# Performance work log

Hardware: AMD Instinct MI355X
Metric: run time of the kernel (lower is better)

Reference implementation:

```python
import jax, jax.numpy as jnp
import numpy as np

N_NODES = 65536
N_EDGES = 1048576
D_IN = 1024
D_HID = 64
N_CLS = 32


def gcn_conv(x, W, b, src, dst, n_nodes):
    """PyG GCNConv: linear transform, then symmetric-normalized aggregation
    with implicit self-loops (fill value 1)."""
    xw = x @ W  # [N, d_out]
    e = src.shape[0]
    # degree over destination index, including the self-loop (+1)
    deg = jax.ops.segment_sum(jnp.ones((e,), xw.dtype), dst, num_segments=n_nodes) + 1.0
    dinv_sqrt = jax.lax.rsqrt(deg)  # deg >= 1, safe
    norm = dinv_sqrt[src] * dinv_sqrt[dst]  # [E]
    agg = jax.ops.segment_sum(xw[src] * norm[:, None], dst, num_segments=n_nodes)
    # self-loop contribution: norm = deg_i^{-1}
    agg = agg + xw * (1.0 / deg)[:, None]
    return agg + b


def setup_inputs() -> dict:
    key = jax.random.key(0)
    k_x, k_e, k_w1, k_b1, k_w2, k_b2 = jax.random.split(key, 6)
    x = jax.random.normal(k_x, (N_NODES, D_IN), dtype=jnp.float32)
    edge_index = jax.random.randint(k_e, (2, N_EDGES), 0, N_NODES, dtype=jnp.int64)
    s1 = 1.0 / np.sqrt(D_IN)
    s2 = 1.0 / np.sqrt(D_HID)
    W1 = jax.random.uniform(k_w1, (D_IN, D_HID), jnp.float32, -s1, s1)
    b1 = jax.random.uniform(k_b1, (D_HID,), jnp.float32, -s1, s1)
    W2 = jax.random.uniform(k_w2, (D_HID, N_CLS), jnp.float32, -s2, s2)
    b2 = jax.random.uniform(k_b2, (N_CLS,), jnp.float32, -s2, s2)
    return {"x": x, "edge_index": edge_index, "W1": W1, "b1": b1, "W2": W2, "b2": b2}


def reference(x, edge_index, W1, b1, W2, b2):
    src, dst = edge_index[0], edge_index[1]
    n = x.shape[0]
    h = gcn_conv(x, W1, b1, src, dst, n)
    h = jax.nn.relu(h)
    # dropout is identity in eval mode
    h = gcn_conv(h, W2, b2, src, dst, n)
    return jax.nn.log_softmax(h, axis=1)
```

## Files before the change

### kernel.cpp

```cpp
#include <hip/hip_runtime.h>
#include <hip/hip_bf16.h>

#define N_NODES 65536
#define D_IN 1024
#define D_HID 64
#define N_CLS 32
#define CPAD 5

typedef short short8 __attribute__((ext_vector_type(8)));
typedef float floatx4 __attribute__((ext_vector_type(4)));

__device__ __forceinline__ unsigned short f2bf(float f) {
  union { float f; unsigned u; } cv; cv.f = f;
  unsigned r = (cv.u + 0x7FFFu + ((cv.u >> 16) & 1u)) >> 16;
  return (unsigned short)r;
}
__device__ __forceinline__ float2 bf2f2(unsigned v) {
  union { unsigned u; float f; } a, b;
  a.u = v << 16;
  b.u = v & 0xFFFF0000u;
  return make_float2(a.f, b.f);
}

__global__ void k_count_w1t(const int* __restrict__ dst, int* __restrict__ cnt,
                            const float* __restrict__ w1, unsigned short* __restrict__ w1t,
                            int e4) {
  int b = blockIdx.x;
  if (b >= 1024) {
    int i = (b - 1024) * 256 + threadIdx.x;
    int k = i / D_HID, n = i % D_HID;
    w1t[n * D_IN + k] = f2bf(w1[i]);
    return;
  }
  int i = b * 256 + threadIdx.x;
  if (i < e4) {
    int4 d = ((const int4*)dst)[i];
    atomicAdd(&cnt[d.x << CPAD], 1);
    atomicAdd(&cnt[d.y << CPAD], 1);
    atomicAdd(&cnt[d.z << CPAD], 1);
    atomicAdd(&cnt[d.w << CPAD], 1);
  }
}

__global__ void k_scan_a(const int* __restrict__ cnt, int* __restrict__ bsum) {
  __shared__ int s[256];
  int t = threadIdx.x;
  s[t] = cnt[(blockIdx.x * 256 + t) << CPAD];
  __syncthreads();
  for (int off = 128; off > 0; off >>= 1) {
    if (t < off) s[t] += s[t + off];
    __syncthreads();
  }
  if (t == 0) bsum[blockIdx.x] = s[0];
}

__global__ void k_scan_c(const int* __restrict__ cnt, const int* __restrict__ bsum,
                         int* __restrict__ rowptr, int* __restrict__ cursor,
                         float* __restrict__ dinv) {
  __shared__ int s[256];
  int t = threadIdx.x;
  s[t] = (t < blockIdx.x) ? bsum[t] : 0;
  __syncthreads();
  for (int off = 128; off > 0; off >>= 1) {
    if (t < off) s[t] += s[t + off];
    __syncthreads();
  }
  int blockoff = s[0];
  __syncthreads();
  int i = blockIdx.x * 256 + t;
  int v = cnt[i << CPAD];
  s[t] = v;
  __syncthreads();
  for (int off = 1; off < 256; off <<= 1) {
    int x = (t >= off) ? s[t - off] : 0;
    __syncthreads();
    s[t] += x;
    __syncthreads();
  }
  int excl = s[t] - v + blockoff;
  rowptr[i] = excl;
  cursor[i << CPAD] = excl;
  dinv[i] = rsqrtf((float)(v + 1));
  if (i == N_NODES - 1) rowptr[N_NODES] = excl + v;
}

__global__ __launch_bounds__(256) void k_fill_gemm1(
    const int* __restrict__ src, const int* __restrict__ dst,
    int* __restrict__ cursor, int* __restrict__ csr_src, int e4,
    const float* __restrict__ x, const unsigned short* __restrict__ w1t,
    const float* __restrict__ dinv, unsigned short* __restrict__ xw1s) {
  if (blockIdx.x >= 1024) {
    int i = (blockIdx.x - 1024) * 256 + threadIdx.x;
    int e8 = e4 >> 1;
    if (i < e8) {
      const int4* d4 = (const int4*)dst;
      const int4* s4 = (const int4*)src;
      int4 da = d4[2 * i], db = d4[2 * i + 1];
      int4 sa = s4[2 * i], sb = s4[2 * i + 1];
      int p0 = atomicAdd(&cursor[da.x << CPAD], 1);
      int p1 = atomicAdd(&cursor[da.y << CPAD], 1);
      int p2 = atomicAdd(&cursor[da.z << CPAD], 1);
      int p3 = atomicAdd(&cursor[da.w << CPAD], 1);
      int p4 = atomicAdd(&cursor[db.x << CPAD], 1);
      int p5 = atomicAdd(&cursor[db.y << CPAD], 1);
      int p6 = atomicAdd(&cursor[db.z << CPAD], 1);
      int p7 = atomicAdd(&cursor[db.w << CPAD], 1);
      csr_src[p0] = sa.x; csr_src[p1] = sa.y;
      csr_src[p2] = sa.z; csr_src[p3] = sa.w;
      csr_src[p4] = sb.x; csr_src[p5] = sb.y;
      csr_src[p6] = sb.z; csr_src[p7] = sb.w;
    }
    return;
  }
  int wave = threadIdx.x >> 6;
  int lane = threadIdx.x & 63;
  int quad = lane >> 4;
  int l16 = lane & 15;
  int rowbase = blockIdx.x * 64 + wave * 16;
  const float* xrow = x + (size_t)(rowbase + l16) * D_IN + quad * 8;
  const unsigned short* bbase = w1t + quad * 8;
  floatx4 acc[4];
#pragma unroll
  for (int nt = 0; nt < 4; nt++) acc[nt] = (floatx4){0.f, 0.f, 0.f, 0.f};
  float4 p0 = *(const float4*)(xrow + 0);
  float4 p1 = *(const float4*)(xrow + 4);
  float4 p2 = *(const float4*)(xrow + 32);
  float4 p3 = *(const float4*)(xrow + 36);
  short8 bf0[4], bf1[4];
#pragma unroll
  for (int nt = 0; nt < 4; nt++) {
    const unsigned short* bp = bbase + (size_t)(nt * 16 + l16) * D_IN;
    bf0[nt] = *(const short8*)(bp);
    bf1[nt] = *(const short8*)(bp + 32);
  }
  for (int k0 = 0; k0 < D_IN; k0 += 64) {
    float4 c0 = p0, c1 = p1, c2 = p2, c3 = p3;
    int kn = (k0 + 64 < D_IN) ? k0 + 64 : k0;
    p0 = *(const float4*)(xrow + kn);
    p1 = *(const float4*)(xrow + kn + 4);
    p2 = *(const float4*)(xrow + kn + 32);
    p3 = *(const float4*)(xrow + kn + 36);
    float av0[8] = {c0.x, c0.y, c0.z, c0.w, c1.x, c1.y, c1.z, c1.w};
    float av1[8] = {c2.x, c2.y, c2.z, c2.w, c3.x, c3.y, c3.z, c3.w};
    short8 af0, af1;
    unsigned* u0 = (unsigned*)&af0;
    unsigned* u1 = (unsigned*)&af1;
#pragma unroll
    for (int j = 0; j < 4; j++) {
      asm("v_cvt_pk_bf16_f32 %0, %1, %2" : "=v"(u0[j]) : "v"(av0[2 * j]), "v"(av0[2 * j + 1]));
      asm("v_cvt_pk_bf16_f32 %0, %1, %2" : "=v"(u1[j]) : "v"(av1[2 * j]), "v"(av1[2 * j + 1]));
    }
#pragma unroll
    for (int nt = 0; nt < 4; nt++)
      acc[nt] = __builtin_amdgcn_mfma_f32_16x16x32_bf16(af0, bf0[nt], acc[nt], 0, 0, 0);
#pragma unroll
    for (int nt = 0; nt < 4; nt++)
      bf0[nt] = *(const short8*)(bbase + (size_t)(nt * 16 + l16) * D_IN + kn);
#pragma unroll
    for (int nt = 0; nt < 4; nt++)
      acc[nt] = __builtin_amdgcn_mfma_f32_16x16x32_bf16(af1, bf1[nt], acc[nt], 0, 0, 0);
#pragma unroll
    for (int nt = 0; nt < 4; nt++)
      bf1[nt] = *(const short8*)(bbase + (size_t)(nt * 16 + l16) * D_IN + kn + 32);
  }
#pragma unroll
  for (int r = 0; r < 4; r++) {
    int row = rowbase + quad * 4 + r;
    float sc = dinv[row];
#pragma unroll
    for (int nt = 0; nt < 4; nt++)
      xw1s[(size_t)row * D_HID + nt * 16 + l16] = f2bf(acc[nt][r] * sc);
  }
}

__global__ __launch_bounds__(256) void k_agg1(const unsigned* __restrict__ xw1s2,
    const int* __restrict__ rowptr, const int* __restrict__ csr_src,
    const float* __restrict__ dinv, const float* __restrict__ b1,
    const float* __restrict__ w2, unsigned short* __restrict__ xw2s) {
  __shared__ float w2s[D_HID * N_CLS];
  for (int i = threadIdx.x; i < D_HID * N_CLS; i += 256) w2s[i] = w2[i];
  __syncthreads();
  int wave = threadIdx.x >> 6;
  int lane = threadIdx.x & 63;
  int h = lane >> 5, l = lane & 31;
  int node = blockIdx.x * 4 + wave;
  float dd = dinv[node];
  int beg = rowptr[node], end = rowptr[node + 1];
  float cx[8], cy[8];
#pragma unroll
  for (int j = 0; j < 8; j++) { cx[j] = 0.f; cy[j] = 0.f; }
  for (int e = beg + h; e < end; e += 16) {
    int idx[8]; bool val[8];
#pragma unroll
    for (int j = 0; j < 8; j++) {
      int ee = e + 2 * j;
      val[j] = ee < end;
      idx[j] = csr_src[val[j] ? ee : beg];
    }
#pragma unroll
    for (int j = 0; j < 8; j++) {
      float2 v = bf2f2(xw1s2[(size_t)idx[j] * 32 + l]);
      cx[j] += val[j] ? v.x : 0.f;
      cy[j] += val[j] ? v.y : 0.f;
    }
  }
  float sx = ((cx[0] + cx[1]) + (cx[2] + cx[3])) + ((cx[4] + cx[5]) + (cx[6] + cx[7]));
  float sy = ((cy[0] + cy[1]) + (cy[2] + cy[3])) + ((cy[4] + cy[5]) + (cy[6] + cy[7]));
  sx += __shfl_xor(sx, 32);
  sy += __shfl_xor(sy, 32);
  float2 self = bf2f2(xw1s2[(size_t)node * 32 + l]);
  float2 bb = ((const float2*)b1)[l];
  float vx = dd * (sx + self.x) + bb.x;
  float vy = dd * (sy + self.y) + bb.y;
  vx = vx > 0.f ? vx : 0.f;
  vy = vy > 0.f ? vy : 0.f;
  int c = lane & 31;
  float p = 0.f;
#pragma unroll
  for (int kk = 0; kk < 32; kk++) {
    int k = h * 32 + kk;
    float hv = (k & 1) ? __shfl(vy, k >> 1) : __shfl(vx, k >> 1);
    p += hv * w2s[k * N_CLS + c];
  }
  p += __shfl_xor(p, 32);
  if (lane < 32) xw2s[(size_t)node * N_CLS + c] = f2bf(p * dd);
}

__global__ __launch_bounds__(256) void k_agg2(const unsigned* __restrict__ xw2s2,
    const int* __restrict__ rowptr, const int* __restrict__ csr_src,
    const float* __restrict__ dinv, const float* __restrict__ b2,
    float* __restrict__ out) {
  int wave = threadIdx.x >> 6;
  int lane = threadIdx.x & 63;
  int q = lane >> 4, l = lane & 15;
  int node = blockIdx.x * 4 + wave;
  float dd = dinv[node];
  int beg = rowptr[node], end = rowptr[node + 1];
  float cx[4], cy[4];
#pragma unroll
  for (int j = 0; j < 4; j++) { cx[j] = 0.f; cy[j] = 0.f; }
  for (int e = beg + q; e < end; e += 16) {
    int idx[4]; bool val[4];
#pragma unroll
    for (int j = 0; j < 4; j++) {
      int ee = e + 4 * j;
      val[j] = ee < end;
      idx[j] = csr_src[val[j] ? ee : beg];
    }
#pragma unroll
    for (int j = 0; j < 4; j++) {
      float2 v = bf2f2(xw2s2[(size_t)idx[j] * 16 + l]);
      cx[j] += val[j] ? v.x : 0.f;
      cy[j] += val[j] ? v.y : 0.f;
    }
  }
  float sx = (cx[0] + cx[1]) + (cx[2] + cx[3]);
  float sy = (cy[0] + cy[1]) + (cy[2] + cy[3]);
  sx += __shfl_xor(sx, 32); sy += __shfl_xor(sy, 32);
  sx += __shfl_xor(sx, 16); sy += __shfl_xor(sy, 16);
  float2 self = bf2f2(xw2s2[(size_t)node * 16 + l]);
  float2 bb = ((const float2*)b2)[l];
  float lx = dd * (sx + self.x) + bb.x;
  float ly = dd * (sy + self.y) + bb.y;
  float m = fmaxf(lx, ly);
#pragma unroll
  for (int o = 8; o > 0; o >>= 1) m = fmaxf(m, __shfl_xor(m, o));
  float s2 = __expf(lx - m) + __expf(ly - m);
#pragma unroll
  for (int o = 8; o > 0; o >>= 1) s2 += __shfl_xor(s2, o);
  float lse = m + __logf(s2);
  if (lane < 16)
    ((float2*)out)[(size_t)node * 16 + l] = make_float2(lx - lse, ly - lse);
}

extern "C" void kernel_launch(void* const* d_in, const int* in_sizes, int n_in,
                              void* d_out, int out_size, void* d_ws, size_t ws_size,
                              hipStream_t stream) {
  (void)n_in; (void)out_size; (void)ws_size;
  const float* x  = (const float*)d_in[0];
  const int*   ei = (const int*)d_in[1];
  const float* w1 = (const float*)d_in[2];
  const float* b1 = (const float*)d_in[3];
  const float* w2 = (const float*)d_in[4];
  const float* b2 = (const float*)d_in[5];
  float* out = (float*)d_out;
  int e = in_sizes[1] / 2;
  const int* src = ei;
  const int* dst = ei + e;

  char* ws = (char*)d_ws;
  int* cnt            = (int*)(ws + 0x0000000);
  int* cursor         = (int*)(ws + 0x0800000);
  int* rowptr         = (int*)(ws + 0x1000000);
  float* dinv         = (float*)(ws + 0x1050000);
  int* bsum           = (int*)(ws + 0x1090000);
  int* csr_src        = (int*)(ws + 0x10A0000);
  unsigned short* w1t = (unsigned short*)(ws + 0x14A0000);
  unsigned short* xw1s= (unsigned short*)(ws + 0x14C0000);
  unsigned short* xw2s= (unsigned short*)(ws + 0x1CC0000);

  int e4 = e / 4;
  hipMemsetAsync(cnt, 0, (size_t)N_NODES * 32 * sizeof(int), stream);
  k_count_w1t<<<1280, 256, 0, stream>>>(dst, cnt, w1, w1t, e4);
  k_scan_a   <<<N_NODES / 256, 256, 0, stream>>>(cnt, bsum);
  k_scan_c   <<<N_NODES / 256, 256, 0, stream>>>(cnt, bsum, rowptr, cursor, dinv);
  k_fill_gemm1<<<1536, 256, 0, stream>>>(src, dst, cursor, csr_src, e4,
                                         x, w1t, dinv, xw1s);
  k_agg1     <<<N_NODES / 4, 256, 0, stream>>>((const unsigned*)xw1s, rowptr, csr_src,
                                               dinv, b1, w2, xw2s);
  k_agg2     <<<N_NODES / 4, 256, 0, stream>>>((const unsigned*)xw2s, rowptr, csr_src,
                                               dinv, b2, out);
}
```

Before: 549.1 us.

## Build CSR with two-level bucketed counting sort using shared-memory atomics

Replaces the global-atomic degree count and cursor-based CSR fill with a two-pass bucket sort. Edges are histogrammed by the high bits of dst into 256 buckets using per-block shared-memory atomics, then scattered as packed (dst low byte, src) words. A per-bucket kernel then builds rowptr, dinv and csr_src locally. This removes the large padded counter memset and the contended random global atomics. In exchange the CSR build now takes more kernel launches, and the first GEMM no longer overlaps with the edge fill. Packing src into 16 bits relies on there being at most 65536 nodes.

Measured after the change: 493.9 us. -10.1%, faster.

```diff
diff --git a/kernel.cpp b/kernel.cpp
--- a/kernel.cpp
+++ b/kernel.cpp
@@ -5,7 +5,8 @@
 #define D_IN 1024
 #define D_HID 64
 #define N_CLS 32
-#define CPAD 5
+#define NBUK 256
+#define NEB 1024
 
 typedef short short8 __attribute__((ext_vector_type(8)));
 typedef float floatx4 __attribute__((ext_vector_type(4)));
@@ -22,53 +23,55 @@
   return make_float2(a.f, b.f);
 }
 
-__global__ void k_count_w1t(const int* __restrict__ dst, int* __restrict__ cnt,
-                            const float* __restrict__ w1, unsigned short* __restrict__ w1t,
-                            int e4) {
+__global__ void k_hist(const int* __restrict__ dst, int* __restrict__ H,
+                       const float* __restrict__ w1, unsigned short* __restrict__ w1t,
+                       int e4) {
   int b = blockIdx.x;
-  if (b >= 1024) {
-    int i = (b - 1024) * 256 + threadIdx.x;
+  if (b >= NEB) {
+    int i = (b - NEB) * 256 + threadIdx.x;
     int k = i / D_HID, n = i % D_HID;
     w1t[n * D_IN + k] = f2bf(w1[i]);
     return;
   }
-  int i = b * 256 + threadIdx.x;
-  if (i < e4) {
-    int4 d = ((const int4*)dst)[i];
-    atomicAdd(&cnt[d.x << CPAD], 1);
-    atomicAdd(&cnt[d.y << CPAD], 1);
-    atomicAdd(&cnt[d.z << CPAD], 1);
-    atomicAdd(&cnt[d.w << CPAD], 1);
-  }
-}
-
-__global__ void k_scan_a(const int* __restrict__ cnt, int* __restrict__ bsum) {
+  __shared__ int hist[NBUK];
+  int t = threadIdx.x;
+  hist[t] = 0;
+  __syncthreads();
+  int i4 = b * 256 + t;
+  if (i4 < e4) {
+    int4 d = ((const int4*)dst)[i4];
+    atomicAdd(&hist[d.x >> 8], 1);
+    atomicAdd(&hist[d.y >> 8], 1);
+    atomicAdd(&hist[d.z >> 8], 1);
+    atomicAdd(&hist[d.w >> 8], 1);
+  }
+  __syncthreads();
+  H[t * NEB + b] = hist[t];
+}
+
+__global__ void k_scan_bucket(int* __restrict__ H, int* __restrict__ btot) {
+  int bin = blockIdx.x, t = threadIdx.x;
+  int4 v = ((int4*)(H + bin * NEB))[t];
+  int s0 = v.x, s1 = s0 + v.y, s2 = s1 + v.z, s3 = s2 + v.w;
+  __shared__ int s[256];
+  s[t] = s3;
+  __syncthreads();
+  for (int off = 1; off < 256; off <<= 1) {
+    int x = (t >= off) ? s[t - off] : 0;
+    __syncthreads();
+    s[t] += x;
+    __syncthreads();
+  }
+  int excl = s[t] - s3;
+  ((int4*)(H + bin * NEB))[t] = make_int4(excl, excl + s0, excl + s1, excl + s2);
+  if (t == 255) btot[bin] = excl + s3;
+}
+
+__global__ void k_scan_tot(const int* __restrict__ btot, int* __restrict__ btoff,
+                           int* __restrict__ rowptr, int e) {
   __shared__ int s[256];
   int t = threadIdx.x;
-  s[t] = cnt[(blockIdx.x * 256 + t) << CPAD];
-  __syncthreads();
-  for (int off = 128; off > 0; off >>= 1) {
-    if (t < off) s[t] += s[t + off];
-    __syncthreads();
-  }
-  if (t == 0) bsum[blockIdx.x] = s[0];
-}
-
-__global__ void k_scan_c(const int* __restrict__ cnt, const int* __restrict__ bsum,
-                         int* __restrict__ rowptr, int* __restrict__ cursor,
-                         float* __restrict__ dinv) {
-  __shared__ int s[256];
-  int t = threadIdx.x;
-  s[t] = (t < blockIdx.x) ? bsum[t] : 0;
-  __syncthreads();
-  for (int off = 128; off > 0; off >>= 1) {
-    if (t < off) s[t] += s[t + off];
-    __syncthreads();
-  }
-  int blockoff = s[0];
-  __syncthreads();
-  int i = blockIdx.x * 256 + t;
-  int v = cnt[i << CPAD];
+  int v = btot[t];
   s[t] = v;
   __syncthreads();
   for (int off = 1; off < 256; off <<= 1) {
@@ -77,41 +80,68 @@
     s[t] += x;
     __syncthreads();
   }
-  int excl = s[t] - v + blockoff;
-  rowptr[i] = excl;
-  cursor[i << CPAD] = excl;
-  dinv[i] = rsqrtf((float)(v + 1));
-  if (i == N_NODES - 1) rowptr[N_NODES] = excl + v;
-}
-
-__global__ __launch_bounds__(256) void k_fill_gemm1(
-    const int* __restrict__ src, const int* __restrict__ dst,
-    int* __restrict__ cursor, int* __restrict__ csr_src, int e4,
+  btoff[t] = s[t] - v;
+  if (t == 0) rowptr[N_NODES] = e;
+}
+
+__global__ void k_scatter(const int* __restrict__ dst, const int* __restrict__ src,
+                          const int* __restrict__ H, const int* __restrict__ btoff,
+                          unsigned* __restrict__ pk, int e4) {
+  __shared__ int cur[NBUK];
+  int b = blockIdx.x, t = threadIdx.x;
+  cur[t] = btoff[t] + H[t * NEB + b];
+  __syncthreads();
+  int i4 = b * 256 + t;
+  if (i4 < e4) {
+    int4 d = ((const int4*)dst)[i4];
+    int4 sv = ((const int4*)src)[i4];
+    int p0 = atomicAdd(&cur[d.x >> 8], 1);
+    int p1 = atomicAdd(&cur[d.y >> 8], 1);
+    int p2 = atomicAdd(&cur[d.z >> 8], 1);
+    int p3 = atomicAdd(&cur[d.w >> 8], 1);
+    pk[p0] = ((unsigned)(d.x & 255) << 16) | (unsigned)sv.x;
+    pk[p1] = ((unsigned)(d.y & 255) << 16) | (unsigned)sv.y;
+    pk[p2] = ((unsigned)(d.z & 255) << 16) | (unsigned)sv.z;
+    pk[p3] = ((unsigned)(d.w & 255) << 16) | (unsigned)sv.w;
+  }
+}
+
+__global__ void k_bucket_csr(const unsigned* __restrict__ pk, const int* __restrict__ btoff,
+                             const int* __restrict__ btot, int* __restrict__ rowptr,
+                             int* __restrict__ csr_src, float* __restrict__ dinv) {
+  __shared__ int cnt[NBUK], sc[NBUK], cur[NBUK];
+  int bin = blockIdx.x, t = threadIdx.x;
+  cnt[t] = 0;
+  __syncthreads();
+  int beg = btoff[bin], len = btot[bin];
+  for (int i = t; i < len; i += 256)
+    atomicAdd(&cnt[(pk[beg + i] >> 16) & 255], 1);
+  __syncthreads();
+  int c = cnt[t];
+  sc[t] = c;
+  __syncthreads();
+  for (int off = 1; off < 256; off <<= 1) {
+    int x = (t >= off) ? sc[t - off] : 0;
+    __syncthreads();
+    sc[t] += x;
+    __syncthreads();
+  }
+  int excl = sc[t] - c;
+  int node = bin * 256 + t;
+  rowptr[node] = beg + excl;
+  dinv[node] = rsqrtf((float)(c + 1));
+  cur[t] = excl;
+  __syncthreads();
+  for (int i = t; i < len; i += 256) {
+    unsigned u = pk[beg + i];
+    int p = atomicAdd(&cur[(u >> 16) & 255], 1);
+    csr_src[beg + p] = (int)(u & 0xFFFFu);
+  }
+}
+
+__global__ __launch_bounds__(256) void k_gemm1(
     const float* __restrict__ x, const unsigned short* __restrict__ w1t,
     const float* __restrict__ dinv, unsigned short* __restrict__ xw1s) {
-  if (blockIdx.x >= 1024) {
-    int i = (blockIdx.x - 1024) * 256 + threadIdx.x;
-    int e8 = e4 >> 1;
-    if (i < e8) {
-      const int4* d4 = (const int4*)dst;
-      const int4* s4 = (const int4*)src;
-      int4 da = d4[2 * i], db = d4[2 * i + 1];
-      int4 sa = s4[2 * i], sb = s4[2 * i + 1];
-      int p0 = atomicAdd(&cursor[da.x << CPAD], 1);
-      int p1 = atomicAdd(&cursor[da.y << CPAD], 1);
-      int p2 = atomicAdd(&cursor[da.z << CPAD], 1);
-      int p3 = atomicAdd(&cursor[da.w << CPAD], 1);
-      int p4 = atomicAdd(&cursor[db.x << CPAD], 1);
-      int p5 = atomicAdd(&cursor[db.y << CPAD], 1);
-      int p6 = atomicAdd(&cursor[db.z << CPAD], 1);
-      int p7 = atomicAdd(&cursor[db.w << CPAD], 1);
-      csr_src[p0] = sa.x; csr_src[p1] = sa.y;
-      csr_src[p2] = sa.z; csr_src[p3] = sa.w;
-      csr_src[p4] = sb.x; csr_src[p5] = sb.y;
-      csr_src[p6] = sb.z; csr_src[p7] = sb.w;
-    }
-    return;
-  }
   int wave = threadIdx.x >> 6;
   int lane = threadIdx.x & 63;
   int quad = lane >> 4;
@@ -289,25 +319,26 @@
   const int* dst = ei + e;
 
   char* ws = (char*)d_ws;
-  int* cnt            = (int*)(ws + 0x0000000);
-  int* cursor         = (int*)(ws + 0x0800000);
-  int* rowptr         = (int*)(ws + 0x1000000);
-  float* dinv         = (float*)(ws + 0x1050000);
-  int* bsum           = (int*)(ws + 0x1090000);
-  int* csr_src        = (int*)(ws + 0x10A0000);
-  unsigned short* w1t = (unsigned short*)(ws + 0x14A0000);
-  unsigned short* xw1s= (unsigned short*)(ws + 0x14C0000);
-  unsigned short* xw2s= (unsigned short*)(ws + 0x1CC0000);
+  int* H              = (int*)(ws + 0x0000000);
+  int* btot           = (int*)(ws + 0x0100000);
+  int* btoff          = (int*)(ws + 0x0100400);
+  int* rowptr         = (int*)(ws + 0x0101000);
+  float* dinv         = (float*)(ws + 0x0150000);
+  unsigned* pk        = (unsigned*)(ws + 0x0200000);
+  int* csr_src        = (int*)(ws + 0x0600000);
+  unsigned short* w1t = (unsigned short*)(ws + 0x0A00000);
+  unsigned short* xw1s= (unsigned short*)(ws + 0x0A20000);
+  unsigned short* xw2s= (unsigned short*)(ws + 0x1220000);
 
   int e4 = e / 4;
-  hipMemsetAsync(cnt, 0, (size_t)N_NODES * 32 * sizeof(int), stream);
-  k_count_w1t<<<1280, 256, 0, stream>>>(dst, cnt, w1, w1t, e4);
-  k_scan_a   <<<N_NODES / 256, 256, 0, stream>>>(cnt, bsum);
-  k_scan_c   <<<N_NODES / 256, 256, 0, stream>>>(cnt, bsum, rowptr, cursor, dinv);
-  k_fill_gemm1<<<1536, 256, 0, stream>>>(src, dst, cursor, csr_src, e4,
-                                         x, w1t, dinv, xw1s);
-  k_agg1     <<<N_NODES / 4, 256, 0, stream>>>((const unsigned*)xw1s, rowptr, csr_src,
-                                               dinv, b1, w2, xw2s);
-  k_agg2     <<<N_NODES / 4, 256, 0, stream>>>((const unsigned*)xw2s, rowptr, csr_src,
-                                               dinv, b2, out);
-}
+  k_hist       <<<NEB + 256, 256, 0, stream>>>(dst, H, w1, w1t, e4);
+  k_scan_bucket<<<NBUK, 256, 0, stream>>>(H, btot);
+  k_scan_tot   <<<1, 256, 0, stream>>>(btot, btoff, rowptr, e);
+  k_scatter    <<<NEB, 256, 0, stream>>>(dst, src, H, btoff, pk, e4);
+  k_bucket_csr <<<NBUK, 256, 0, stream>>>(pk, btoff, btot, rowptr, csr_src, dinv);
+  k_gemm1      <<<N_NODES / 64, 256, 0, stream>>>(x, w1t, dinv, xw1s);
+  k_agg1       <<<N_NODES / 4, 256, 0, stream>>>((const unsigned*)xw1s, rowptr, csr_src,
+                                                 dinv, b1, w2, xw2s);
+  k_agg2       <<<N_NODES / 4, 256, 0, stream>>>((const unsigned*)xw2s, rowptr, csr_src,
+                                                 dinv, b2, out);
+}
```
